# Kernel tuning notes

Measured on AMD Instinct MI355X. Metric: run time of the kernel, lower is better.

## Reference

```python
import jax, jax.numpy as jnp
import numpy as np


def get_grid_index(init_grid_size, map_size):
    # nearest-neighbor 'interpolation' of flat indices, matching F.interpolate(mode='nearest')
    H_init, W_init = init_grid_size
    H, W = map_size
    # torch nearest: src index = floor(dst * scale), scale = src/dst
    rows = jnp.floor(jnp.arange(H_init) * (H / H_init)).astype(jnp.int32)
    cols = jnp.floor(jnp.arange(W_init) * (W / W_init)).astype(jnp.int32)
    idx = rows[:, None] * W + cols[None, :]
    return idx.reshape(-1)  # [N_init]


def _map2token(feature_map, idx_token, N, H_init, W_init):
    B, C, H, W = feature_map.shape
    N_init = H_init * W_init
    idx_hw = get_grid_index((H_init, W_init), (H, W))  # [N_init]
    # gather per-grid feature values: fm_flat[b, idx_hw] -> [B, N_init, C]
    fm = feature_map.transpose(0, 2, 3, 1).reshape(B, H * W, C)
    src = fm[:, idx_hw, :]  # [B, N_init, C]
    # scatter-add into tokens with counts
    def scatter_b(src_b, idx_b):
        num = jnp.zeros((N, C), src_b.dtype).at[idx_b].add(src_b)
        cnt = jnp.zeros((N,), src_b.dtype).at[idx_b].add(1.0)
        return num / (cnt + 1e-6)[:, None]
    return jax.vmap(scatter_b)(src, idx_token)  # [B, N, C]


def _token2map(x, idx_token, H, W, H_init, W_init):
    B, N, C = x.shape
    N_init = H_init * W_init
    idx_hw = get_grid_index((H_init, W_init), (H, W))  # [N_init]
    # each initial grid point contributes token x[b, idx_token[b,i]] to map cell idx_hw[i]
    def scatter_b(x_b, idx_tok_b):
        src = x_b[idx_tok_b]  # [N_init, C]
        num = jnp.zeros((H * W, C), x_b.dtype).at[idx_hw].add(src)
        cnt = jnp.zeros((H * W,), x_b.dtype).at[idx_hw].add(1.0)
        return num / (cnt + 1e-6)[:, None]
    out = jax.vmap(scatter_b)(x, idx_token)  # [B, H*W, C]
    return out.reshape(B, H, W, C).transpose(0, 3, 1, 2)


def setup_inputs() -> dict:
    key = jax.random.key(0)
    k1, k2, k3 = jax.random.split(key, 3)
    B, C, H, W = 8, 256, 56, 56
    N = 784
    H_init = W_init = 56
    N_init = H_init * W_init
    feature_map = jax.random.normal(k1, (B, C, H, W), dtype=jnp.float32)
    x = jax.random.normal(k2, (B, N, C), dtype=jnp.float32)
    idx_token = jax.random.randint(k3, (B, N_init), 0, N)
    return {"feature_map": feature_map, "x": x, "idx_token": idx_token,
            "token_num": N, "map_H": H, "map_W": W, "init_H": H_init, "init_W": W_init}


def reference(feature_map, x, idx_token, token_num, map_H, map_W, init_H, init_W):
    tokens = _map2token(feature_map, idx_token, token_num, init_H, init_W)
    fmap = _token2map(x, idx_token, map_H, map_W, init_H, init_W)
    return tokens, fmap
```

## Files before the change

kernel.cpp:

```cpp
#include <hip/hip_runtime.h>

#define BATCH 8
#define CCH   256
#define HWSZ  3136
#define NTOK  784
#define NINIT 3136
#define MAXM  64

#define FMT_OFF   0
#define CNT_OFF   25690112
#define SLOT_OFF  25715200

#define TRANS_BLOCKS (BATCH * 49 * 4)
#define FMAP_BLOCKS  (BATCH * 49 * 4)
#define CSR_BLOCKS   BATCH
#define K1_BLOCKS    (TRANS_BLOCKS + FMAP_BLOCKS + CSR_BLOCKS)
#define TOK_BLOCKS   (BATCH * NTOK)

__global__ __launch_bounds__(256) void prep_kernel(
    const float* __restrict__ fm,
    const float* __restrict__ x,
    const int*   __restrict__ idx,
    float*       __restrict__ fmap,
    float*       __restrict__ fmT,
    int*         __restrict__ cnt,
    int*         __restrict__ slot)
{
    __shared__ __align__(16) float tile[64][65];
    const int bid = blockIdx.x;
    const int tid = threadIdx.x;

    if (bid < TRANS_BLOCKS) {
        const int b  = bid & 7;
        int t = bid >> 3;
        const int ct = t & 3;
        const int it = t >> 2;
        const int c0 = ct * 64;
        const int i0 = it * 64;

        const int q  = tid & 15;
        const int r0 = tid >> 4;

        #pragma unroll
        for (int p = 0; p < 4; ++p) {
            const int r = r0 + p * 16;
            const float4 v = *(const float4*)&fm[((size_t)(b * CCH + c0 + r)) * HWSZ + i0 + q * 4];
            tile[r][q * 4 + 0] = v.x;
            tile[r][q * 4 + 1] = v.y;
            tile[r][q * 4 + 2] = v.z;
            tile[r][q * 4 + 3] = v.w;
        }
        __syncthreads();
        #pragma unroll
        for (int p = 0; p < 4; ++p) {
            const int i = r0 + p * 16;
            float4 w;
            w.x = tile[q * 4 + 0][i];
            w.y = tile[q * 4 + 1][i];
            w.z = tile[q * 4 + 2][i];
            w.w = tile[q * 4 + 3][i];
            *(float4*)&fmT[((size_t)(b * HWSZ + i0 + i)) * CCH + c0 + q * 4] = w;
        }
    } else if (bid < TRANS_BLOCKS + FMAP_BLOCKS) {
        int t = bid - TRANS_BLOCKS;
        const int b  = t & 7;  t >>= 3;
        const int ct = t & 3;  t >>= 2;
        const int it = t;
        const int i0 = it * 64;
        const int c0 = ct * 64;

        __shared__ int ns[64];
        const int lane = tid & 63;
        const int rr   = tid >> 6;

        if (tid < 64) ns[tid] = idx[b * NINIT + i0 + tid];
        __syncthreads();

        const int q  = tid & 15;
        const int r0 = tid >> 4;
        #pragma unroll
        for (int p = 0; p < 4; ++p) {
            const int r = r0 + p * 16;
            const float4 v = *(const float4*)&x[((size_t)b * NTOK + ns[r]) * CCH + c0 + q * 4];
            tile[r][q * 4 + 0] = v.x;
            tile[r][q * 4 + 1] = v.y;
            tile[r][q * 4 + 2] = v.z;
            tile[r][q * 4 + 3] = v.w;
        }
        __syncthreads();

        const float inv = 1.0f / (1.0f + 1e-6f);
        float* outb = fmap + (size_t)b * CCH * HWSZ;
        #pragma unroll
        for (int cc = rr; cc < 64; cc += 4) {
            outb[(size_t)(c0 + cc) * HWSZ + i0 + lane] = tile[lane][cc] * inv;
        }
    } else {
        const int b = bid - (TRANS_BLOCKS + FMAP_BLOCKS);
        for (int i = tid; i < NINIT; i += 256) {
            const int n = idx[b * NINIT + i];
            const int p = atomicAdd(&cnt[b * NTOK + n], 1);
            if (p < MAXM) slot[(b * NTOK + n) * MAXM + p] = i;
        }
    }
}

__global__ __launch_bounds__(256) void tokens_kernel(
    const float* __restrict__ fmT,
    const int*   __restrict__ cnt,
    const int*   __restrict__ slot,
    float*       __restrict__ tokens)
{
    const int bid = blockIdx.x;
    const int tid = threadIdx.x;
    const int b = bid & 7;
    const int n = bid >> 3;

    __shared__ int list[MAXM];
    const int mraw = cnt[b * NTOK + n];
    const int m = mraw < MAXM ? mraw : MAXM;
    if (tid < m) list[tid] = slot[(b * NTOK + n) * MAXM + tid];
    __syncthreads();

    const float* base = fmT + (size_t)b * HWSZ * CCH + tid;
    float s = 0.0f;
    for (int k = 0; k < m; ++k) s += base[(size_t)list[k] * CCH];

    tokens[((size_t)b * NTOK + n) * CCH + tid] = s / ((float)mraw + 1e-6f);
}

extern "C" void kernel_launch(void* const* d_in, const int* in_sizes, int n_in,
                              void* d_out, int out_size, void* d_ws, size_t ws_size,
                              hipStream_t stream) {
    const float* fm  = (const float*)d_in[0];
    const float* x   = (const float*)d_in[1];
    const int*   idx = (const int*)d_in[2];

    float* tokens = (float*)d_out;
    float* fmap   = (float*)d_out + (size_t)BATCH * NTOK * CCH;

    char* ws   = (char*)d_ws;
    float* fmT = (float*)(ws + FMT_OFF);
    int*   cnt = (int*)(ws + CNT_OFF);
    int*   slot= (int*)(ws + SLOT_OFF);

    hipMemsetAsync(cnt, 0, BATCH * NTOK * sizeof(int), stream);
    prep_kernel<<<K1_BLOCKS, 256, 0, stream>>>(fm, x, idx, fmap, fmT, cnt, slot);
    tokens_kernel<<<TOK_BLOCKS, 256, 0, stream>>>(fmT, cnt, slot, tokens);
}
```

Before: 115.8 us.

## Build CSR in shared memory, drop memset, coarsen blocks, vectorize token gather

The per-batch CSR build now counts and assigns slots with shared-memory atomics, so the separate memset launch of the global count array is no longer needed. The transpose and fmap scatter blocks each loop over all four channel tiles instead of using one block per tile, cutting the grid by four. The token gather kernel processes eight tokens per block with float4 loads and no shared-list sync. Slot capacity drops from 64 to 40, which silently truncates any token with more than 40 members, and fewer blocks in the first kernel may reduce the memory parallelism available.

```diff
diff --git a/kernel.cpp b/kernel.cpp
--- a/kernel.cpp
+++ b/kernel.cpp
@@ -5,19 +5,18 @@
 #define HWSZ  3136
 #define NTOK  784
 #define NINIT 3136
-#define MAXM  64
+#define MAXM  40
 
 #define FMT_OFF   0
 #define CNT_OFF   25690112
-#define SLOT_OFF  25715200
+#define SLOT_OFF  (25690112 + 25600)
 
-#define TRANS_BLOCKS (BATCH * 49 * 4)
-#define FMAP_BLOCKS  (BATCH * 49 * 4)
-#define CSR_BLOCKS   BATCH
-#define K1_BLOCKS    (TRANS_BLOCKS + FMAP_BLOCKS + CSR_BLOCKS)
-#define TOK_BLOCKS   (BATCH * NTOK)
+#define CSR_BLOCKS 8
+#define TR_BLOCKS  (BATCH * 49)
+#define FM_BLOCKS  (BATCH * 49)
+#define D1_BLOCKS  (CSR_BLOCKS + TR_BLOCKS + FM_BLOCKS)
 
-__global__ __launch_bounds__(256) void prep_kernel(
+__global__ __launch_bounds__(256) void d1_kernel(
     const float* __restrict__ fm,
     const float* __restrict__ x,
     const int*   __restrict__ idx,
@@ -27,85 +26,95 @@
     int*         __restrict__ slot)
 {
     __shared__ __align__(16) float tile[64][65];
+    __shared__ int ns[64];
+
     const int bid = blockIdx.x;
     const int tid = threadIdx.x;
 
-    if (bid < TRANS_BLOCKS) {
-        const int b  = bid & 7;
-        int t = bid >> 3;
-        const int ct = t & 3;
-        const int it = t >> 2;
-        const int c0 = ct * 64;
+    if (bid < CSR_BLOCKS) {
+        int* cnt_s = (int*)tile;
+        int* cur_s = ((int*)tile) + NTOK;
+        const int b = bid;
+        for (int n = tid; n < NTOK; n += 256) { cnt_s[n] = 0; cur_s[n] = 0; }
+        __syncthreads();
+        const int* ib = idx + b * NINIT;
+        for (int i = tid; i < NINIT; i += 256) atomicAdd(&cnt_s[ib[i]], 1);
+        __syncthreads();
+        for (int n = tid; n < NTOK; n += 256) cnt[b * NTOK + n] = cnt_s[n];
+        for (int i = tid; i < NINIT; i += 256) {
+            const int n = ib[i];
+            const int p = atomicAdd(&cur_s[n], 1);
+            if (p < MAXM) slot[(b * NTOK + n) * MAXM + p] = i;
+        }
+    } else if (bid < CSR_BLOCKS + TR_BLOCKS) {
+        int t = bid - CSR_BLOCKS;
+        const int b  = t & 7;
+        const int it = t >> 3;
         const int i0 = it * 64;
-
         const int q  = tid & 15;
         const int r0 = tid >> 4;
 
-        #pragma unroll
-        for (int p = 0; p < 4; ++p) {
-            const int r = r0 + p * 16;
-            const float4 v = *(const float4*)&fm[((size_t)(b * CCH + c0 + r)) * HWSZ + i0 + q * 4];
-            tile[r][q * 4 + 0] = v.x;
-            tile[r][q * 4 + 1] = v.y;
-            tile[r][q * 4 + 2] = v.z;
-            tile[r][q * 4 + 3] = v.w;
+        for (int ct = 0; ct < 4; ++ct) {
+            const int c0 = ct * 64;
+            #pragma unroll
+            for (int p = 0; p < 4; ++p) {
+                const int r = r0 + p * 16;
+                const float4 v = *(const float4*)&fm[((size_t)(b * CCH + c0 + r)) * HWSZ + i0 + q * 4];
+                tile[r][q * 4 + 0] = v.x;
+                tile[r][q * 4 + 1] = v.y;
+                tile[r][q * 4 + 2] = v.z;
+                tile[r][q * 4 + 3] = v.w;
+            }
+            __syncthreads();
+            #pragma unroll
+            for (int p = 0; p < 4; ++p) {
+                const int i = r0 + p * 16;
+                float4 w;
+                w.x = tile[q * 4 + 0][i];
+                w.y = tile[q * 4 + 1][i];
+                w.z = tile[q * 4 + 2][i];
+                w.w = tile[q * 4 + 3][i];
+                *(float4*)&fmT[((size_t)(b * HWSZ + i0 + i)) * CCH + c0 + q * 4] = w;
+            }
+            __syncthreads();
         }
-        __syncthreads();
-        #pragma unroll
-        for (int p = 0; p < 4; ++p) {
-            const int i = r0 + p * 16;
-            float4 w;
-            w.x = tile[q * 4 + 0][i];
-            w.y = tile[q * 4 + 1][i];
-            w.z = tile[q * 4 + 2][i];
-            w.w = tile[q * 4 + 3][i];
-            *(float4*)&fmT[((size_t)(b * HWSZ + i0 + i)) * CCH + c0 + q * 4] = w;
-        }
-    } else if (bid < TRANS_BLOCKS + FMAP_BLOCKS) {
-        int t = bid - TRANS_BLOCKS;
-        const int b  = t & 7;  t >>= 3;
-        const int ct = t & 3;  t >>= 2;
-        const int it = t;
+    } else {
+        int t = bid - CSR_BLOCKS - TR_BLOCKS;
+        const int b  = t & 7;
+        const int it = t >> 3;
         const int i0 = it * 64;
-        const int c0 = ct * 64;
-
-        __shared__ int ns[64];
         const int lane = tid & 63;
         const int rr   = tid >> 6;
+        const int q  = tid & 15;
+        const int r0 = tid >> 4;
 
         if (tid < 64) ns[tid] = idx[b * NINIT + i0 + tid];
         __syncthreads();
 
-        const int q  = tid & 15;
-        const int r0 = tid >> 4;
-        #pragma unroll
-        for (int p = 0; p < 4; ++p) {
-            const int r = r0 + p * 16;
-            const float4 v = *(const float4*)&x[((size_t)b * NTOK + ns[r]) * CCH + c0 + q * 4];
-            tile[r][q * 4 + 0] = v.x;
-            tile[r][q * 4 + 1] = v.y;
-            tile[r][q * 4 + 2] = v.z;
-            tile[r][q * 4 + 3] = v.w;
-        }
-        __syncthreads();
-
-        const float inv = 1.0f / (1.0f + 1e-6f);
+        const float invc = 1.0f / (1.0f + 1e-6f);
         float* outb = fmap + (size_t)b * CCH * HWSZ;
-        #pragma unroll
-        for (int cc = rr; cc < 64; cc += 4) {
-            outb[(size_t)(c0 + cc) * HWSZ + i0 + lane] = tile[lane][cc] * inv;
-        }
-    } else {
-        const int b = bid - (TRANS_BLOCKS + FMAP_BLOCKS);
-        for (int i = tid; i < NINIT; i += 256) {
-            const int n = idx[b * NINIT + i];
-            const int p = atomicAdd(&cnt[b * NTOK + n], 1);
-            if (p < MAXM) slot[(b * NTOK + n) * MAXM + p] = i;
+        for (int ct = 0; ct < 4; ++ct) {
+            const int c0 = ct * 64;
+            #pragma unroll
+            for (int p = 0; p < 4; ++p) {
+                const int r = r0 + p * 16;
+                const float4 v = *(const float4*)&x[((size_t)(b * NTOK + ns[r])) * CCH + c0 + q * 4];
+                tile[r][q * 4 + 0] = v.x;
+                tile[r][q * 4 + 1] = v.y;
+                tile[r][q * 4 + 2] = v.z;
+                tile[r][q * 4 + 3] = v.w;
+            }
+            __syncthreads();
+            #pragma unroll
+            for (int cc = rr; cc < 64; cc += 4) {
+                outb[(size_t)(c0 + cc) * HWSZ + i0 + lane] = tile[lane][cc] * invc;
+            }
+            __syncthreads();
         }
     }
 }
 
-__global__ __launch_bounds__(256) void tokens_kernel(
+__global__ __launch_bounds__(256) void d2_kernel(
     const float* __restrict__ fmT,
     const int*   __restrict__ cnt,
     const int*   __restrict__ slot,
@@ -113,20 +122,27 @@
 {
     const int bid = blockIdx.x;
     const int tid = threadIdx.x;
-    const int b = bid & 7;
-    const int n = bid >> 3;
+    const int b  = bid & 7;
+    const int g  = bid >> 3;
+    const int tl = tid >> 6;
+    const int c4 = (tid & 63) * 4;
 
-    __shared__ int list[MAXM];
-    const int mraw = cnt[b * NTOK + n];
-    const int m = mraw < MAXM ? mraw : MAXM;
-    if (tid < m) list[tid] = slot[(b * NTOK + n) * MAXM + tid];
-    __syncthreads();
-
-    const float* base = fmT + (size_t)b * HWSZ * CCH + tid;
-    float s = 0.0f;
-    for (int k = 0; k < m; ++k) s += base[(size_t)list[k] * CCH];
-
-    tokens[((size_t)b * NTOK + n) * CCH + tid] = s / ((float)mraw + 1e-6f);
+    const float* fb = fmT + (size_t)b * HWSZ * CCH;
+    #pragma unroll
+    for (int u = 0; u < 2; ++u) {
+        const int n  = g * 8 + u * 4 + tl;
+        const int m  = cnt[b * NTOK + n];
+        const int mm = m < MAXM ? m : MAXM;
+        const int* sl = slot + (size_t)(b * NTOK + n) * MAXM;
+        float4 acc = {0.f, 0.f, 0.f, 0.f};
+        for (int k = 0; k < mm; ++k) {
+            const float4 v = *(const float4*)&fb[(size_t)sl[k] * CCH + c4];
+            acc.x += v.x; acc.y += v.y; acc.z += v.z; acc.w += v.w;
+        }
+        const float s = 1.0f / ((float)m + 1e-6f);
+        acc.x *= s; acc.y *= s; acc.z *= s; acc.w *= s;
+        *(float4*)&tokens[((size_t)(b * NTOK + n)) * CCH + c4] = acc;
+    }
 }
 
 extern "C" void kernel_launch(void* const* d_in, const int* in_sizes, int n_in,
@@ -139,12 +155,11 @@
     float* tokens = (float*)d_out;
     float* fmap   = (float*)d_out + (size_t)BATCH * NTOK * CCH;
 
-    char* ws   = (char*)d_ws;
-    float* fmT = (float*)(ws + FMT_OFF);
-    int*   cnt = (int*)(ws + CNT_OFF);
-    int*   slot= (int*)(ws + SLOT_OFF);
+    char*  ws   = (char*)d_ws;
+    float* fmT  = (float*)(ws + FMT_OFF);
+    int*   cnt  = (int*)(ws + CNT_OFF);
+    int*   slot = (int*)(ws + SLOT_OFF);
 
-    hipMemsetAsync(cnt, 0, BATCH * NTOK * sizeof(int), stream);
-    prep_kernel<<<K1_BLOCKS, 256, 0, stream>>>(fm, x, idx, fmap, fmT, cnt, slot);
-    tokens_kernel<<<TOK_BLOCKS, 256, 0, stream>>>(fmT, cnt, slot, tokens);
+    d1_kernel<<<D1_BLOCKS, 256, 0, stream>>>(fm, x, idx, fmap, fmT, cnt, slot);
+    d2_kernel<<<BATCH * (NTOK / 8), 256, 0, stream>>>(fmT, cnt, slot, tokens);
 }
```

After: 114.1 us. No clear change (-1.5%).
